# Kernel optimization log

Hardware: AMD Instinct MI355X
Metric: run time of the kernel (lower is better)

The kernel has to match this reference:

```python
import jax, jax.numpy as jnp
import numpy as np

S, B, H, E, L, V = 64, 64, 512, 512, 2, 32000


def setup_inputs() -> dict:
    key = jax.random.key(0)
    ks = jax.random.split(key, 10)
    k = 1.0 / np.sqrt(H)
    return {
        "tokens": jax.random.randint(ks[0], (S, B), 0, V),
        "hidden": jnp.zeros((L, B, H), jnp.float32),
        "emb": jax.random.uniform(ks[1], (V, E), jnp.float32, -0.1, 0.1),
        "Wr": jax.random.uniform(ks[2], (L, E + H, H), jnp.float32, -k, k),
        "br": jax.random.uniform(ks[3], (L, H), jnp.float32, -k, k),
        "Wz": jax.random.uniform(ks[4], (L, E + H, H), jnp.float32, -k, k),
        "bz": jax.random.uniform(ks[5], (L, H), jnp.float32, -k, k),
        "Wh": jax.random.uniform(ks[6], (L, E + H, H), jnp.float32, -k, k),
        "bh": jax.random.uniform(ks[7], (L, H), jnp.float32, -k, k),
        "Wout": jax.random.uniform(ks[8], (H, V), jnp.float32, -0.1, 0.1),
        "bout": jnp.zeros((V,), jnp.float32),
    }


def reference(tokens, hidden, emb, Wr, br, Wz, bz, Wh, bh, Wout, bout):
    # tokens: [S,B] int; hidden: [L,B,H]
    x = emb[tokens]  # [S,B,E]  (dropout is identity: dp_keep_prob=1)

    def step(h, x_t):  # h: [L,B,H], x_t: [B,E]
        inp = x_t
        new_h = []
        for l in range(L):
            cat = jnp.concatenate([inp, h[l]], axis=-1)  # [B, E+H]
            r = jax.nn.sigmoid(cat @ Wr[l] + br[l])
            z = jax.nn.sigmoid(cat @ Wz[l] + bz[l])
            cat_h = jnp.concatenate([inp, r * h[l]], axis=-1)
            hh = jnp.tanh(cat_h @ Wh[l] + bh[l])
            nh = (1.0 - z) * h[l] + z * hh
            new_h.append(nh)
            inp = nh
        h_new = jnp.stack(new_h)  # [L,B,H]
        logits_t = inp @ Wout + bout  # [B,V]
        return h_new, logits_t

    hidden_final, logits = jax.lax.scan(step, hidden, x)
    return logits, hidden_final  # [S,B,V], [L,B,H]
```

## Files before the change

kernel.cpp:

```cpp
#include <hip/hip_runtime.h>
#include <hip/hip_bf16.h>
#include <math.h>

#define S_ 64
#define B_ 64
#define H_ 512
#define E_ 512
#define L_ 2
#define V_ 32000

#define SB_   (S_*B_)
#define SBE_  (S_*B_*E_)
#define SBH_  (S_*B_*H_)
#define BH_   (B_*H_)
#define KP_   1536

typedef _Float16 f16x8 __attribute__((ext_vector_type(8)));
typedef _Float16 f16x4 __attribute__((ext_vector_type(4)));
typedef float    f32x4 __attribute__((ext_vector_type(4)));

__global__ __launch_bounds__(256) void embed_k(const int* __restrict__ tok,
                                               const float* __restrict__ emb,
                                               float* __restrict__ x) {
    int idx = blockIdx.x * 256 + threadIdx.x;
    int e4 = idx & (E_/4 - 1);
    int sb = idx >> 7;
    int tk = tok[sb];
    *(float4*)(x + (size_t)sb * E_ + e4 * 4) =
        *(const float4*)(emb + (size_t)tk * E_ + e4 * 4);
}

__global__ __launch_bounds__(256) void gemm_bias(
    const float* __restrict__ A, int lda,
    const float* __restrict__ W, int ldw,
    const float* __restrict__ bias,
    float* __restrict__ C, int ldc,
    int K) {
    __shared__ float As[16][68];
    __shared__ float Bs[16][68];

    const int tid = threadIdx.x;
    const int tx = tid & 15;
    const int ty = tid >> 4;
    const int n0 = blockIdx.x * 64;
    const int m0 = blockIdx.y * 64;

    float acc[4][4] = {};

    for (int k0 = 0; k0 < K; k0 += 16) {
        {
            int i  = tid >> 2;
            int j4 = tid & 3;
            const float4 av = *(const float4*)(A + (size_t)(m0 + i) * lda + k0 + j4 * 4);
            As[j4 * 4 + 0][i] = av.x;
            As[j4 * 4 + 1][i] = av.y;
            As[j4 * 4 + 2][i] = av.z;
            As[j4 * 4 + 3][i] = av.w;
        }
        {
            int r  = tid >> 4;
            int c4 = tid & 15;
            *(float4*)(&Bs[r][c4 * 4]) =
                *(const float4*)(W + (size_t)(k0 + r) * ldw + n0 + c4 * 4);
        }
        __syncthreads();
        #pragma unroll
        for (int kk = 0; kk < 16; kk++) {
            float4 a4 = *(float4*)(&As[kk][ty * 4]);
            float4 b4 = *(float4*)(&Bs[kk][tx * 4]);
            acc[0][0] += a4.x * b4.x; acc[0][1] += a4.x * b4.y; acc[0][2] += a4.x * b4.z; acc[0][3] += a4.x * b4.w;
            acc[1][0] += a4.y * b4.x; acc[1][1] += a4.y * b4.y; acc[1][2] += a4.y * b4.z; acc[1][3] += a4.y * b4.w;
            acc[2][0] += a4.z * b4.x; acc[2][1] += a4.z * b4.y; acc[2][2] += a4.z * b4.z; acc[2][3] += a4.z * b4.w;
            acc[3][0] += a4.w * b4.x; acc[3][1] += a4.w * b4.y; acc[3][2] += a4.w * b4.z; acc[3][3] += a4.w * b4.w;
        }
        __syncthreads();
    }

    float4 bv = *(const float4*)(bias + n0 + tx * 4);
    #pragma unroll
    for (int i = 0; i < 4; i++) {
        int row = m0 + ty * 4 + i;
        float4 out;
        out.x = acc[i][0] + bv.x;
        out.y = acc[i][1] + bv.y;
        out.z = acc[i][2] + bv.z;
        out.w = acc[i][3] + bv.w;
        *(float4*)(C + (size_t)row * ldc + n0 + tx * 4) = out;
    }
}

__device__ __forceinline__ float sigmoidf_(float xv) {
    float e = __expf(-fabsf(xv));
    float s = 1.f / (1.f + e);
    return xv >= 0.f ? s : 1.f - s;
}

__global__ __launch_bounds__(256) void rz_step(
    const float* __restrict__ Pr_t, const float* __restrict__ Pz_t,
    const float* __restrict__ Wr_hid, const float* __restrict__ Wz_hid,
    const float* __restrict__ h_prev,
    float* __restrict__ zbuf, float* __restrict__ rhbuf) {
    __shared__ float hs[64][132];
    const int bid = blockIdx.x;
    const int g = bid >> 5;
    const int ct = bid & 31;
    const int tid = threadIdx.x;
    const int c = ct * 16 + (tid & 15);
    const int bg = tid >> 4;

    const float* Wg = g ? Wz_hid : Wr_hid;
    const float* P  = g ? Pz_t   : Pr_t;

    float acc[4] = {0.f, 0.f, 0.f, 0.f};

    for (int kk = 0; kk < H_; kk += 128) {
        #pragma unroll
        for (int q = 0; q < 8; q++) {
            int idx = q * 256 + tid;
            int row = idx >> 5;
            int c4  = idx & 31;
            *(float4*)(&hs[row][c4 * 4]) =
                *(const float4*)(h_prev + row * H_ + kk + c4 * 4);
        }
        __syncthreads();
        const float* Wp = Wg + (size_t)kk * H_ + c;
        #pragma unroll 4
        for (int k = 0; k < 128; k++) {
            float w = Wp[(size_t)k * H_];
            #pragma unroll
            for (int i = 0; i < 4; i++)
                acc[i] += w * hs[bg * 4 + i][k];
        }
        __syncthreads();
    }

    #pragma unroll
    for (int i = 0; i < 4; i++) {
        int b = bg * 4 + i;
        float pre = P[b * H_ + c] + acc[i];
        float v = sigmoidf_(pre);
        if (g == 0) rhbuf[b * H_ + c] = v * h_prev[b * H_ + c];
        else        zbuf[b * H_ + c]  = v;
    }
}

__global__ __launch_bounds__(256) void hh_step(
    const float* __restrict__ Ph_t,
    const float* __restrict__ Wh_hid,
    const float* __restrict__ rh,
    const float* __restrict__ h_prev,
    const float* __restrict__ zbuf,
    float* __restrict__ h_out) {
    __shared__ float hs[64][132];
    const int ct = blockIdx.x;
    const int tid = threadIdx.x;
    const int c = ct * 16 + (tid & 15);
    const int bg = tid >> 4;

    float acc[4] = {0.f, 0.f, 0.f, 0.f};

    for (int kk = 0; kk < H_; kk += 128) {
        #pragma unroll
        for (int q = 0; q < 8; q++) {
            int idx = q * 256 + tid;
            int row = idx >> 5;
            int c4  = idx & 31;
            *(float4*)(&hs[row][c4 * 4]) =
                *(const float4*)(rh + row * H_ + kk + c4 * 4);
        }
        __syncthreads();
        const float* Wp = Wh_hid + (size_t)kk * H_ + c;
        #pragma unroll 4
        for (int k = 0; k < 128; k++) {
            float w = Wp[(size_t)k * H_];
            #pragma unroll
            for (int i = 0; i < 4; i++)
                acc[i] += w * hs[bg * 4 + i][k];
        }
        __syncthreads();
    }

    #pragma unroll
    for (int i = 0; i < 4; i++) {
        int b = bg * 4 + i;
        float pre = Ph_t[b * H_ + c] + acc[i];
        float hhv = tanhf(pre);
        float z = zbuf[b * H_ + c];
        float h = h_prev[b * H_ + c];
        h_out[b * H_ + c] = (1.f - z) * h + z * hhv;
    }
}

__global__ __launch_bounds__(256) void castA_k(const float* __restrict__ in,
                                               _Float16* __restrict__ A2) {
    int idx = blockIdx.x * 256 + threadIdx.x;
    int m = idx >> 7;
    int q = idx & 127;
    float4 xv = *(const float4*)(in + (size_t)m * H_ + q * 4);
    float xs[4] = {xv.x, xv.y, xv.z, xv.w};
    f16x4 hi, lo, sc;
    #pragma unroll
    for (int i = 0; i < 4; i++) {
        _Float16 ah = (_Float16)xs[i];
        float ahf = (float)ah;
        hi[i] = ah;
        lo[i] = (_Float16)((xs[i] - ahf) * 32.0f);
        sc[i] = (_Float16)(ahf * 0.0625f);
    }
    _Float16* row = A2 + (size_t)m * KP_ + q * 4;
    *(f16x4*)(row)        = hi;
    *(f16x4*)(row + 512)  = lo;
    *(f16x4*)(row + 1024) = sc;
}

__global__ __launch_bounds__(256) void castB_k(const float* __restrict__ W,
                                               _Float16* __restrict__ Bt) {
    __shared__ float ws[64][68];
    const int v0 = blockIdx.x * 64;
    const int h0 = blockIdx.y * 64;
    const int tid = threadIdx.x;

    #pragma unroll
    for (int q = 0; q < 4; q++) {
        int idx = q * 256 + tid;
        int h  = idx >> 4;
        int v4 = idx & 15;
        *(float4*)(&ws[h][v4 * 4]) =
            *(const float4*)(W + (size_t)(h0 + h) * V_ + v0 + v4 * 4);
    }
    __syncthreads();

    const int v  = tid >> 2;
    const int hq = tid & 3;
    #pragma unroll
    for (int j = 0; j < 2; j++) {
        int hb = j * 32 + hq * 8;
        f16x8 hi, lo, sc;
        #pragma unroll
        for (int i = 0; i < 8; i++) {
            float wv = ws[hb + i][v];
            _Float16 bh = (_Float16)wv;
            float bhf = (float)bh;
            hi[i] = bh;
            sc[i] = (_Float16)(bhf * 0.03125f);
            lo[i] = (_Float16)((wv - bhf) * 16.0f);
        }
        _Float16* row = Bt + (size_t)(v0 + v) * KP_ + h0 + hb;
        *(f16x8*)(row)        = hi;
        *(f16x8*)(row + 512)  = sc;
        *(f16x8*)(row + 1024) = lo;
    }
}

__global__ __launch_bounds__(256) void gemm_logits(
    const _Float16* __restrict__ Ag,
    const _Float16* __restrict__ Bg,
    const float* __restrict__ bias,
    float* __restrict__ C) {
    __shared__ __align__(16) _Float16 As[128 * 64];
    __shared__ __align__(16) _Float16 Bs[128 * 64];

    const int tid  = threadIdx.x;
    const int lane = tid & 63;
    const int w    = tid >> 6;
    const int n0   = blockIdx.x * 128;
    const int m0   = blockIdx.y * 128;
    const int wm   = (w >> 1) * 64;
    const int wn   = (w & 1) * 64;

    f32x4 acc[4][4];
    #pragma unroll
    for (int i = 0; i < 4; i++)
        #pragma unroll
        for (int j = 0; j < 4; j++)
            acc[i][j] = (f32x4){0.f, 0.f, 0.f, 0.f};

    const int grow  = lane >> 3;
    const int gslot = (lane & 7) ^ grow;

    for (int kt = 0; kt < KP_ / 64; ++kt) {
        const int k0 = kt * 64;
        #pragma unroll
        for (int q = 0; q < 4; ++q) {
            int ch  = w * 4 + q;
            int row = ch * 8 + grow;
            const _Float16* ga = Ag + (size_t)(m0 + row) * KP_ + k0 + gslot * 8;
            const _Float16* gb = Bg + (size_t)(n0 + row) * KP_ + k0 + gslot * 8;
            __builtin_amdgcn_global_load_lds(
                (const __attribute__((address_space(1))) void*)ga,
                (__attribute__((address_space(3))) void*)(As + ch * 512), 16, 0, 0);
            __builtin_amdgcn_global_load_lds(
                (const __attribute__((address_space(1))) void*)gb,
                (__attribute__((address_space(3))) void*)(Bs + ch * 512), 16, 0, 0);
        }
        __syncthreads();

        #pragma unroll
        for (int ks = 0; ks < 2; ++ks) {
            f16x8 af[4], bf[4];
            #pragma unroll
            for (int i = 0; i < 4; ++i) {
                int arow  = wm + i * 16 + (lane & 15);
                int aslot = (ks * 4 + (lane >> 4)) ^ (arow & 7);
                af[i] = *(const f16x8*)(As + arow * 64 + aslot * 8);
                int brow  = wn + i * 16 + (lane & 15);
                int bslot = (ks * 4 + (lane >> 4)) ^ (brow & 7);
                bf[i] = *(const f16x8*)(Bs + brow * 64 + bslot * 8);
            }
            #pragma unroll
            for (int mi = 0; mi < 4; ++mi)
                #pragma unroll
                for (int nj = 0; nj < 4; ++nj)
                    acc[mi][nj] = __builtin_amdgcn_mfma_f32_16x16x32_f16(
                        af[mi], bf[nj], acc[mi][nj], 0, 0, 0);
        }
        __syncthreads();
    }

    #pragma unroll
    for (int nj = 0; nj < 4; ++nj) {
        int col = n0 + wn + nj * 16 + (lane & 15);
        float bv = bias[col];
        #pragma unroll
        for (int mi = 0; mi < 4; ++mi) {
            int rb = m0 + wm + mi * 16 + (lane >> 4) * 4;
            #pragma unroll
            for (int j = 0; j < 4; ++j)
                C[(size_t)(rb + j) * V_ + col] = acc[mi][nj][j] + bv;
        }
    }
}

extern "C" void kernel_launch(void* const* d_in, const int* in_sizes, int n_in,
                              void* d_out, int out_size, void* d_ws, size_t ws_size,
                              hipStream_t stream) {
    const int*   tokens = (const int*)  d_in[0];
    const float* hidden = (const float*)d_in[1];
    const float* emb    = (const float*)d_in[2];
    const float* Wr     = (const float*)d_in[3];
    const float* br     = (const float*)d_in[4];
    const float* Wz     = (const float*)d_in[5];
    const float* bz     = (const float*)d_in[6];
    const float* Wh     = (const float*)d_in[7];
    const float* bh     = (const float*)d_in[8];
    const float* Wout   = (const float*)d_in[9];
    const float* bout   = (const float*)d_in[10];

    float* out = (float*)d_out;
    float* out_hidden = out + (size_t)SB_ * V_;

    float* ws = (float*)d_ws;
    float* x     = ws;
    float* hseq1 = x + SBE_;
    float* hseq2 = hseq1 + SBH_;
    float* Pr    = hseq2 + SBH_;
    float* Pz    = Pr + SBH_;
    float* Ph    = Pz + SBH_;
    float* zbuf  = Ph + SBH_;
    float* rhbuf = zbuf + BH_;
    _Float16* A2 = (_Float16*)(rhbuf + BH_);
    _Float16* Bt = A2 + (size_t)SB_ * KP_;

    embed_k<<<SBE_ / 4 / 256, 256, 0, stream>>>(tokens, emb, x);

    castB_k<<<dim3(V_ / 64, H_ / 64), 256, 0, stream>>>(Wout, Bt);

    const int WL = (E_ + H_) * H_;
    const float* layer_in[2] = {x, hseq1};
    float* hseqs[2] = {hseq1, hseq2};

    for (int l = 0; l < L_; l++) {
        const float* A = layer_in[l];
        const float* Wr_l = Wr + (size_t)l * WL;
        const float* Wz_l = Wz + (size_t)l * WL;
        const float* Wh_l = Wh + (size_t)l * WL;

        dim3 gpre(H_ / 64, SB_ / 64);
        gemm_bias<<<gpre, 256, 0, stream>>>(A, E_, Wr_l, H_, br + l * H_, Pr, H_, E_);
        gemm_bias<<<gpre, 256, 0, stream>>>(A, E_, Wz_l, H_, bz + l * H_, Pz, H_, E_);
        gemm_bias<<<gpre, 256, 0, stream>>>(A, E_, Wh_l, H_, bh + l * H_, Ph, H_, E_);

        const float* Wr_hid = Wr_l + (size_t)E_ * H_;
        const float* Wz_hid = Wz_l + (size_t)E_ * H_;
        const float* Wh_hid = Wh_l + (size_t)E_ * H_;

        for (int t = 0; t < S_; t++) {
            const float* h_prev = (t == 0) ? (hidden + (size_t)l * BH_)
                                           : (hseqs[l] + (size_t)(t - 1) * BH_);
            rz_step<<<64, 256, 0, stream>>>(Pr + (size_t)t * BH_, Pz + (size_t)t * BH_,
                                            Wr_hid, Wz_hid, h_prev, zbuf, rhbuf);
            hh_step<<<32, 256, 0, stream>>>(Ph + (size_t)t * BH_, Wh_hid, rhbuf,
                                            h_prev, zbuf, hseqs[l] + (size_t)t * BH_);
        }

        hipMemcpyAsync(out_hidden + (size_t)l * BH_, hseqs[l] + (size_t)(S_ - 1) * BH_,
                       (size_t)BH_ * sizeof(float), hipMemcpyDeviceToDevice, stream);
    }

    castA_k<<<SBE_ / 4 / 256, 256, 0, stream>>>(hseq2, A2);

    gemm_logits<<<dim3(V_ / 128, SB_ / 128), 256, 0, stream>>>(A2, Bt, bout, out);
}
```

Measured before the change: 7.663 ms.

## Fuse per-timestep GRU recurrence into one persistent cooperative kernel with grid sync

Replaces the 128 small rz_step/hh_step launches per layer with a single cooperative kernel of 256 blocks that loops over all timesteps. It uses grid.sync() between the r/z gate phase and the candidate/update phase. Each block now handles 16 batch rows by 16 columns over the full K of 512, so more blocks share the recurrent work. The aim is to remove per-step kernel launch overhead and spread the recurrence across more CUs. The cost is two grid-wide barriers per step, and only half of the blocks do work in the hh phase.

```diff
diff --git a/kernel.cpp b/kernel.cpp
--- a/kernel.cpp
+++ b/kernel.cpp
@@ -1,6 +1,9 @@
 #include <hip/hip_runtime.h>
 #include <hip/hip_bf16.h>
+#include <hip/hip_cooperative_groups.h>
 #include <math.h>
+
+namespace cg = cooperative_groups;
 
 #define S_ 64
 #define B_ 64
@@ -95,99 +98,97 @@
     return xv >= 0.f ? s : 1.f - s;
 }
 
-__global__ __launch_bounds__(256) void rz_step(
-    const float* __restrict__ Pr_t, const float* __restrict__ Pz_t,
+__global__ __launch_bounds__(256) void gru_seq_k(
+    const float* __restrict__ Pr, const float* __restrict__ Pz,
+    const float* __restrict__ Ph,
     const float* __restrict__ Wr_hid, const float* __restrict__ Wz_hid,
-    const float* __restrict__ h_prev,
+    const float* __restrict__ Wh_hid,
+    const float* __restrict__ h0,
+    float* __restrict__ hseq,
     float* __restrict__ zbuf, float* __restrict__ rhbuf) {
-    __shared__ float hs[64][132];
+    cg::grid_group grid = cg::this_grid();
+    __shared__ float hs[16][516];
+
     const int bid = blockIdx.x;
-    const int g = bid >> 5;
+    const int tid = threadIdx.x;
+    const int g  = bid >> 7;
+    const int bt = (bid >> 5) & 3;
     const int ct = bid & 31;
-    const int tid = threadIdx.x;
-    const int c = ct * 16 + (tid & 15);
-    const int bg = tid >> 4;
-
-    const float* Wg = g ? Wz_hid : Wr_hid;
-    const float* P  = g ? Pz_t   : Pr_t;
-
-    float acc[4] = {0.f, 0.f, 0.f, 0.f};
-
-    for (int kk = 0; kk < H_; kk += 128) {
+    const int bl = tid >> 4;
+    const int c  = ct * 16 + (tid & 15);
+    const int b  = bt * 16 + bl;
+    const size_t o = (size_t)b * H_ + c;
+
+    const float* WgA = g ? Wz_hid : Wr_hid;
+
+    for (int t = 0; t < S_; t++) {
+        const float* h_prev = t ? (hseq + (size_t)(t - 1) * BH_) : h0;
+
         #pragma unroll
         for (int q = 0; q < 8; q++) {
             int idx = q * 256 + tid;
-            int row = idx >> 5;
-            int c4  = idx & 31;
+            int row = idx >> 7;
+            int c4  = idx & 127;
             *(float4*)(&hs[row][c4 * 4]) =
-                *(const float4*)(h_prev + row * H_ + kk + c4 * 4);
+                *(const float4*)(h_prev + (size_t)(bt * 16 + row) * H_ + c4 * 4);
         }
         __syncthreads();
-        const float* Wp = Wg + (size_t)kk * H_ + c;
-        #pragma unroll 4
-        for (int k = 0; k < 128; k++) {
-            float w = Wp[(size_t)k * H_];
+        {
+            float acc[4] = {0.f, 0.f, 0.f, 0.f};
+            const float* Wp = WgA + c;
+            const float4* hb4 = (const float4*)&hs[bl][0];
+            #pragma unroll 2
+            for (int k4 = 0; k4 < 32; k4++) {
+                #pragma unroll
+                for (int j = 0; j < 4; j++) {
+                    float4 hv = hb4[j * 32 + k4];
+                    int kb = j * 128 + k4 * 4;
+                    acc[j] += Wp[(size_t)(kb + 0) * H_] * hv.x;
+                    acc[j] += Wp[(size_t)(kb + 1) * H_] * hv.y;
+                    acc[j] += Wp[(size_t)(kb + 2) * H_] * hv.z;
+                    acc[j] += Wp[(size_t)(kb + 3) * H_] * hv.w;
+                }
+            }
+            const float* P = (g ? Pz : Pr) + (size_t)t * BH_;
+            float pre = P[o] + acc[0] + acc[1] + acc[2] + acc[3];
+            float v = sigmoidf_(pre);
+            if (g == 0) rhbuf[o] = v * hs[bl][c];
+            else        zbuf[o]  = v;
+        }
+        grid.sync();
+
+        if (bid < 128) {
             #pragma unroll
-            for (int i = 0; i < 4; i++)
-                acc[i] += w * hs[bg * 4 + i][k];
-        }
-        __syncthreads();
-    }
-
-    #pragma unroll
-    for (int i = 0; i < 4; i++) {
-        int b = bg * 4 + i;
-        float pre = P[b * H_ + c] + acc[i];
-        float v = sigmoidf_(pre);
-        if (g == 0) rhbuf[b * H_ + c] = v * h_prev[b * H_ + c];
-        else        zbuf[b * H_ + c]  = v;
-    }
-}
-
-__global__ __launch_bounds__(256) void hh_step(
-    const float* __restrict__ Ph_t,
-    const float* __restrict__ Wh_hid,
-    const float* __restrict__ rh,
-    const float* __restrict__ h_prev,
-    const float* __restrict__ zbuf,
-    float* __restrict__ h_out) {
-    __shared__ float hs[64][132];
-    const int ct = blockIdx.x;
-    const int tid = threadIdx.x;
-    const int c = ct * 16 + (tid & 15);
-    const int bg = tid >> 4;
-
-    float acc[4] = {0.f, 0.f, 0.f, 0.f};
-
-    for (int kk = 0; kk < H_; kk += 128) {
-        #pragma unroll
-        for (int q = 0; q < 8; q++) {
-            int idx = q * 256 + tid;
-            int row = idx >> 5;
-            int c4  = idx & 31;
-            *(float4*)(&hs[row][c4 * 4]) =
-                *(const float4*)(rh + row * H_ + kk + c4 * 4);
-        }
-        __syncthreads();
-        const float* Wp = Wh_hid + (size_t)kk * H_ + c;
-        #pragma unroll 4
-        for (int k = 0; k < 128; k++) {
-            float w = Wp[(size_t)k * H_];
-            #pragma unroll
-            for (int i = 0; i < 4; i++)
-                acc[i] += w * hs[bg * 4 + i][k];
-        }
-        __syncthreads();
-    }
-
-    #pragma unroll
-    for (int i = 0; i < 4; i++) {
-        int b = bg * 4 + i;
-        float pre = Ph_t[b * H_ + c] + acc[i];
-        float hhv = tanhf(pre);
-        float z = zbuf[b * H_ + c];
-        float h = h_prev[b * H_ + c];
-        h_out[b * H_ + c] = (1.f - z) * h + z * hhv;
+            for (int q = 0; q < 8; q++) {
+                int idx = q * 256 + tid;
+                int row = idx >> 7;
+                int c4  = idx & 127;
+                *(float4*)(&hs[row][c4 * 4]) =
+                    *(const float4*)(rhbuf + (size_t)(bt * 16 + row) * H_ + c4 * 4);
+            }
+            __syncthreads();
+            float acc[4] = {0.f, 0.f, 0.f, 0.f};
+            const float* Wp = Wh_hid + c;
+            const float4* hb4 = (const float4*)&hs[bl][0];
+            #pragma unroll 2
+            for (int k4 = 0; k4 < 32; k4++) {
+                #pragma unroll
+                for (int j = 0; j < 4; j++) {
+                    float4 hv = hb4[j * 32 + k4];
+                    int kb = j * 128 + k4 * 4;
+                    acc[j] += Wp[(size_t)(kb + 0) * H_] * hv.x;
+                    acc[j] += Wp[(size_t)(kb + 1) * H_] * hv.y;
+                    acc[j] += Wp[(size_t)(kb + 2) * H_] * hv.z;
+                    acc[j] += Wp[(size_t)(kb + 3) * H_] * hv.w;
+                }
+            }
+            float pre = Ph[(size_t)t * BH_ + o] + acc[0] + acc[1] + acc[2] + acc[3];
+            float hhv = tanhf(pre);
+            float z  = zbuf[o];
+            float hp = h_prev[o];
+            hseq[(size_t)t * BH_ + o] = (1.f - z) * hp + z * hhv;
+        }
+        grid.sync();
     }
 }
 
@@ -380,17 +381,20 @@
         gemm_bias<<<gpre, 256, 0, stream>>>(A, E_, Wz_l, H_, bz + l * H_, Pz, H_, E_);
         gemm_bias<<<gpre, 256, 0, stream>>>(A, E_, Wh_l, H_, bh + l * H_, Ph, H_, E_);
 
-        const float* Wr_hid = Wr_l + (size_t)E_ * H_;
-        const float* Wz_hid = Wz_l + (size_t)E_ * H_;
-        const float* Wh_hid = Wh_l + (size_t)E_ * H_;
-
-        for (int t = 0; t < S_; t++) {
-            const float* h_prev = (t == 0) ? (hidden + (size_t)l * BH_)
-                                           : (hseqs[l] + (size_t)(t - 1) * BH_);
-            rz_step<<<64, 256, 0, stream>>>(Pr + (size_t)t * BH_, Pz + (size_t)t * BH_,
-                                            Wr_hid, Wz_hid, h_prev, zbuf, rhbuf);
-            hh_step<<<32, 256, 0, stream>>>(Ph + (size_t)t * BH_, Wh_hid, rhbuf,
-                                            h_prev, zbuf, hseqs[l] + (size_t)t * BH_);
+        {
+            const float* a0 = Pr;
+            const float* a1 = Pz;
+            const float* a2 = Ph;
+            const float* a3 = Wr_l + (size_t)E_ * H_;
+            const float* a4 = Wz_l + (size_t)E_ * H_;
+            const float* a5 = Wh_l + (size_t)E_ * H_;
+            const float* a6 = hidden + (size_t)l * BH_;
+            float* a7 = hseqs[l];
+            float* a8 = zbuf;
+            float* a9 = rhbuf;
+            void* cargs[] = {&a0, &a1, &a2, &a3, &a4, &a5, &a6, &a7, &a8, &a9};
+            hipLaunchCooperativeKernel((void*)gru_seq_k, dim3(256), dim3(256),
+                                       cargs, 0, stream);
         }
 
         hipMemcpyAsync(out_hidden + (size_t)l * BH_, hseqs[l] + (size_t)(S_ - 1) * BH_,
```

New measurement: 14.92 ms. 1.95x slower.
